# Performance work log

Measured on AMD Instinct MI355X. Metric: run time of the kernel, lower is better.

Reference implementation:

```python
import jax, jax.numpy as jnp
import numpy as np

N = 100000        # nodes
E = 3200000       # edges (before self loops)
DIN = 128         # dim_input
DOUT = 64         # dim_output
HID = 4           # per-head hidden of conv1
HEADS = 8         # num_in_head
G = 64            # number of graphs in the batch
NEG_SLOPE = 0.2   # PyG GATConv default


def _gat_conv(x, edge_index, W, att_src, att_dst, bias, concat):
    """PyG GATConv (add_self_loops=True, dropout inactive / eval mode)."""
    n = x.shape[0]
    heads, dout = att_src.shape
    h = (x @ W).reshape(n, heads, dout)                  # [N, H, F]
    loop = jnp.arange(n)
    src = jnp.concatenate([edge_index[0], loop])          # [Et]
    dst = jnp.concatenate([edge_index[1], loop])          # [Et]
    a_s = (h * att_src).sum(-1)                           # [N, H]
    a_d = (h * att_dst).sum(-1)                           # [N, H]
    alpha = jax.nn.leaky_relu(a_s[src] + a_d[dst], NEG_SLOPE)   # [Et, H]
    amax = jax.ops.segment_max(alpha, dst, num_segments=n)      # softmax over in-edges
    ex = jnp.exp(alpha - amax[dst])
    denom = jax.ops.segment_sum(ex, dst, num_segments=n)
    w = ex / (denom[dst] + 1e-16)                         # [Et, H]
    out = jax.ops.segment_sum(h[src] * w[:, :, None], dst, num_segments=n)  # [N, H, F]
    out = out.reshape(n, heads * dout) if concat else out.mean(axis=1)
    return out + bias


def setup_inputs() -> dict:
    key = jax.random.key(0)
    ks = jax.random.split(key, 11)
    x = jax.random.normal(ks[0], (N, DIN), jnp.float32)
    edge_index = jax.random.randint(ks[1], (2, E), 0, N)
    batch = jnp.sort(jax.random.randint(ks[2], (N,), 0, G))
    s1 = 1.0 / np.sqrt(DIN)
    W1 = jax.random.uniform(ks[3], (DIN, HEADS * HID), jnp.float32, -s1, s1)
    att_src1 = jax.random.normal(ks[4], (HEADS, HID), jnp.float32) * 0.1
    att_dst1 = jax.random.normal(ks[5], (HEADS, HID), jnp.float32) * 0.1
    b1 = jnp.zeros((HEADS * HID,), jnp.float32)
    s2 = 1.0 / np.sqrt(HEADS * HID)
    W2 = jax.random.uniform(ks[6], (HEADS * HID, DOUT), jnp.float32, -s2, s2)
    att_src2 = jax.random.normal(ks[7], (1, DOUT), jnp.float32) * 0.1
    att_dst2 = jax.random.normal(ks[8], (1, DOUT), jnp.float32) * 0.1
    b2 = jnp.zeros((DOUT,), jnp.float32)
    return {"x": x, "edge_index": edge_index, "batch": batch,
            "W1": W1, "att_src1": att_src1, "att_dst1": att_dst1, "b1": b1,
            "W2": W2, "att_src2": att_src2, "att_dst2": att_dst2, "b2": b2}


def reference(x, edge_index, batch, W1, att_src1, att_dst1, b1,
              W2, att_src2, att_dst2, b2):
    h = _gat_conv(x, edge_index, W1, att_src1, att_dst1, b1, concat=True)
    h = jax.nn.elu(h)
    h = _gat_conv(h, edge_index, W2, att_src2, att_dst2, b2, concat=False)
    # global_mean_pool over batch ids
    sums = jax.ops.segment_sum(h, batch, num_segments=G)          # [G, DOUT]
    counts = jax.ops.segment_sum(jnp.ones((N,), h.dtype), batch, num_segments=G)
    return sums / jnp.maximum(counts, 1.0)[:, None]
```

## Files before the change

### kernel.cpp

```cpp
#include <hip/hip_runtime.h>
#include <math.h>

static constexpr int NN   = 100000;
static constexpr int NE   = 3200000;
static constexpr int ET   = NE + NN;
static constexpr int DIN  = 128;
static constexpr int H1   = 8;
static constexpr int C1   = 32;
static constexpr int DOUT = 64;
static constexpr int NG   = 64;
static constexpr int NB_SCAN = (NN + 255) / 256;
static constexpr int SLAB = (NN + 255) / 256;
static constexpr int NODES_PER_XCD = (NN + 7) / 8;
static constexpr int SC_SLABS = (ET + 255) / 256;

__device__ __forceinline__ float lrelu(float x){ return x > 0.f ? x : 0.2f*x; }
__device__ __forceinline__ float bfl(unsigned int u){ return __uint_as_float(u << 16); }
__device__ __forceinline__ float bfh(unsigned int u){ return __uint_as_float(u & 0xffff0000u); }
__device__ __forceinline__ unsigned short f2bf(float x){
  unsigned int u = __float_as_uint(x);
  u += 0x7fffu + ((u >> 16) & 1u);
  return (unsigned short)(u >> 16);
}

__global__ __launch_bounds__(256) void k_gemm1(const float* __restrict__ x,
                                               const float* __restrict__ W,
                                               const float* __restrict__ as1,
                                               const float* __restrict__ ad1,
                                               unsigned short* __restrict__ h1b,
                                               float* __restrict__ a_s,
                                               float* __restrict__ a_d){
  __shared__ float w[DIN * C1];
  for (int i = threadIdx.x; i < DIN * C1; i += 256) w[i] = W[i];
  __syncthreads();
  int idx = blockIdx.x * 256 + threadIdx.x;
  int n = idx >> 5, j = idx & 31;
  const float* xr = x + (size_t)n * DIN;
  float acc = 0.f;
  #pragma unroll
  for (int k = 0; k < DIN; ++k) acc += xr[k] * w[k * C1 + j];
  h1b[idx] = f2bf(acc);
  float s = acc * as1[j], d = acc * ad1[j];
  s += __shfl_xor(s, 1, 64); s += __shfl_xor(s, 2, 64);
  d += __shfl_xor(d, 1, 64); d += __shfl_xor(d, 2, 64);
  if ((j & 3) == 0){ a_s[n * H1 + (j >> 2)] = s; a_d[n * H1 + (j >> 2)] = d; }
}

__global__ __launch_bounds__(256) void k_init_cnt(int* __restrict__ cnt){
  int n = blockIdx.x * 256 + threadIdx.x;
  if (n < NN) cnt[n] = 1;
}

__global__ __launch_bounds__(256) void k_hist8(const int* __restrict__ ei, int* __restrict__ cnt){
  int xcd = blockIdx.x & 7;
  int e = (blockIdx.x >> 3) * 256 + threadIdx.x;
  int d = ei[NE + e];
  if (d / NODES_PER_XCD == xcd) atomicAdd(&cnt[d], 1);
}

__global__ __launch_bounds__(256) void k_scan_blk(const int* __restrict__ cnt,
                                                  int* __restrict__ tmp, int* __restrict__ btot){
  int g = blockIdx.x * 256 + threadIdx.x;
  int v = (g < NN) ? cnt[g] : 0;
  int lane = threadIdx.x & 63, wv = threadIdx.x >> 6;
  int xv = v;
  #pragma unroll
  for (int o = 1; o < 64; o <<= 1){ int y = __shfl_up(xv, o, 64); if (lane >= o) xv += y; }
  __shared__ int ws[4];
  if (lane == 63) ws[wv] = xv;
  __syncthreads();
  int off = 0;
  for (int i = 0; i < wv; ++i) off += ws[i];
  xv += off;
  if (g < NN) tmp[g] = xv;
  if (threadIdx.x == 255) btot[blockIdx.x] = xv;
}

__global__ __launch_bounds__(512) void k_scan_top(int* __restrict__ btot){
  int t = threadIdx.x;
  int v = (t < NB_SCAN) ? btot[t] : 0;
  int lane = t & 63, wv = t >> 6;
  int xv = v;
  #pragma unroll
  for (int o = 1; o < 64; o <<= 1){ int y = __shfl_up(xv, o, 64); if (lane >= o) xv += y; }
  __shared__ int ws[8];
  if (lane == 63) ws[wv] = xv;
  __syncthreads();
  int off = 0;
  for (int i = 0; i < wv; ++i) off += ws[i];
  xv += off;
  if (t < NB_SCAN) btot[t] = xv - v;
}

__global__ __launch_bounds__(256) void k_scan_fin(const int* __restrict__ cnt,
                                                  const int* __restrict__ tmp,
                                                  const int* __restrict__ btot,
                                                  int* __restrict__ row, int* __restrict__ cur){
  int g = blockIdx.x * 256 + threadIdx.x;
  if (g < NN){
    int ex = tmp[g] - cnt[g] + btot[g >> 8];
    row[g] = ex; cur[g] = ex;
  } else if (g == NN){
    row[NN] = ET;
  }
}

__global__ __launch_bounds__(256) void k_scatter8(const int* __restrict__ ei,
                                                  int* __restrict__ cur, int* __restrict__ ssrc){
  int xcd = blockIdx.x & 7;
  int e = (blockIdx.x >> 3) * 256 + threadIdx.x;
  if (e >= ET) return;
  int s, d;
  if (e < NE) { s = ei[e]; d = ei[NE + e]; }
  else        { s = e - NE; d = s; }
  if (d / NODES_PER_XCD != xcd) return;
  int pos = atomicAdd(&cur[d], 1);
  ssrc[pos] = s;
}

__global__ __launch_bounds__(256, 4) void k_agg1(const int* __restrict__ row,
                                              const int* __restrict__ ssrc,
                                              const float* __restrict__ a_s,
                                              const float* __restrict__ a_d,
                                              const unsigned short* __restrict__ h1b,
                                              const float* __restrict__ b1,
                                              float* __restrict__ out1){
  int node = (blockIdx.x * 256 + threadIdx.x) >> 6;
  int lane = threadIdx.x & 63;
  int l = lane & 7, g = lane >> 3;
  float adv = a_d[node * H1 + l];
  int beg = row[node], end = row[node + 1];
  float a0 = 0.f, a1 = 0.f, a2 = 0.f, a3 = 0.f, den = 0.f;
  for (int base = beg; base < end; base += 64){
    int sv[8]; float liv[8];
    #pragma unroll
    for (int u = 0; u < 8; ++u){
      int k = base + u * 8 + g;
      liv[u] = (k < end) ? 1.f : 0.f;
      sv[u] = ssrc[k < end ? k : end - 1];
    }
    uint2 hraw[8]; float araw[8];
    #pragma unroll
    for (int u = 0; u < 8; ++u){
      hraw[u] = *(const uint2*)(h1b + (size_t)sv[u] * C1 + 4 * l);
      araw[u] = a_s[sv[u] * H1 + l];
    }
    #pragma unroll
    for (int u = 0; u < 8; ++u){
      float al = liv[u] * __expf(lrelu(araw[u] + adv));
      den += al;
      a0 += al * bfl(hraw[u].x); a1 += al * bfh(hraw[u].x);
      a2 += al * bfl(hraw[u].y); a3 += al * bfh(hraw[u].y);
    }
  }
  #pragma unroll
  for (int o = 8; o < 64; o <<= 1){
    den += __shfl_xor(den, o, 64);
    a0 += __shfl_xor(a0, o, 64); a1 += __shfl_xor(a1, o, 64);
    a2 += __shfl_xor(a2, o, 64); a3 += __shfl_xor(a3, o, 64);
  }
  if (g == 0){
    float r = 1.f / den;
    float4 bv = *(const float4*)(b1 + 4 * l);
    float v0 = a0 * r + bv.x, v1 = a1 * r + bv.y, v2 = a2 * r + bv.z, v3 = a3 * r + bv.w;
    v0 = v0 > 0.f ? v0 : expm1f(v0); v1 = v1 > 0.f ? v1 : expm1f(v1);
    v2 = v2 > 0.f ? v2 : expm1f(v2); v3 = v3 > 0.f ? v3 : expm1f(v3);
    *(float4*)(out1 + (size_t)node * C1 + 4 * l) = make_float4(v0, v1, v2, v3);
  }
}

__global__ __launch_bounds__(256) void k_gemm2(const float* __restrict__ hin,
                                               const float* __restrict__ W,
                                               const float* __restrict__ as2,
                                               const float* __restrict__ ad2,
                                               unsigned short* __restrict__ h2b,
                                               float* __restrict__ a_s,
                                               float* __restrict__ a_d){
  __shared__ float w[C1 * DOUT];
  for (int i = threadIdx.x; i < C1 * DOUT; i += 256) w[i] = W[i];
  __syncthreads();
  int idx = blockIdx.x * 256 + threadIdx.x;
  int n = idx >> 6, j = idx & 63;
  const float* hr = hin + (size_t)n * C1;
  float acc = 0.f;
  #pragma unroll
  for (int k = 0; k < C1; ++k) acc += hr[k] * w[k * DOUT + j];
  h2b[idx] = f2bf(acc);
  float s = acc * as2[j], d = acc * ad2[j];
  #pragma unroll
  for (int o = 1; o < 64; o <<= 1){ s += __shfl_xor(s, o, 64); d += __shfl_xor(d, o, 64); }
  if (j == 0){ a_s[n] = s; a_d[n] = d; }
}

__global__ __launch_bounds__(256, 4) void k_agg2(const int* __restrict__ row,
                                              const int* __restrict__ ssrc,
                                              const float* __restrict__ a_s,
                                              const float* __restrict__ a_d,
                                              const unsigned short* __restrict__ h2b,
                                              float* __restrict__ out2){
  int node = (blockIdx.x * 256 + threadIdx.x) >> 6;
  int lane = threadIdx.x & 63;
  int l = lane & 15, g = lane >> 4;
  float adv = a_d[node];
  int beg = row[node], end = row[node + 1];
  float ac0 = 0.f, ac1 = 0.f, ac2 = 0.f, ac3 = 0.f, den = 0.f;
  for (int base = beg; base < end; base += 32){
    int sv[8]; float liv[8];
    #pragma unroll
    for (int u = 0; u < 8; ++u){
      int k = base + u * 4 + g;
      liv[u] = (k < end) ? 1.f : 0.f;
      sv[u] = ssrc[k < end ? k : end - 1];
    }
    uint2 hraw[8]; float asv[8];
    #pragma unroll
    for (int u = 0; u < 8; ++u){
      hraw[u] = *(const uint2*)(h2b + (size_t)sv[u] * DOUT + 4 * l);
      asv[u] = a_s[sv[u]];
    }
    #pragma unroll
    for (int u = 0; u < 8; ++u){
      float al = liv[u] * __expf(lrelu(asv[u] + adv));
      den += al;
      ac0 += al * bfl(hraw[u].x); ac1 += al * bfh(hraw[u].x);
      ac2 += al * bfl(hraw[u].y); ac3 += al * bfh(hraw[u].y);
    }
  }
  #pragma unroll
  for (int o = 16; o < 64; o <<= 1){
    den += __shfl_xor(den, o, 64);
    ac0 += __shfl_xor(ac0, o, 64); ac1 += __shfl_xor(ac1, o, 64);
    ac2 += __shfl_xor(ac2, o, 64); ac3 += __shfl_xor(ac3, o, 64);
  }
  if (g == 0){
    float r = 1.f / den;
    *(float4*)(out2 + (size_t)node * DOUT + 4 * l) =
        make_float4(ac0 * r, ac1 * r, ac2 * r, ac3 * r);
  }
}

__global__ __launch_bounds__(256) void k_bounds(const int* __restrict__ batch,
                                                int* __restrict__ gs){
  int n = blockIdx.x * 256 + threadIdx.x;
  if (n >= NN) return;
  int b = batch[n];
  if (n == 0) gs[b] = 0;
  else if (batch[n - 1] != b) gs[b] = n;
}

__global__ void k_fix(int* __restrict__ gs){
  if (threadIdx.x == 0){
    gs[NG] = NN;
    for (int g = NG - 1; g >= 0; --g) if (gs[g] < 0) gs[g] = gs[g + 1];
  }
}

__global__ __launch_bounds__(256) void k_pool(const float* __restrict__ out2,
                                              const int* __restrict__ batch,
                                              float* __restrict__ sums){
  int start = blockIdx.x * SLAB;
  int stop  = start + SLAB; if (stop > NN) stop = NN;
  int wv = threadIdx.x >> 6, lane = threadIdx.x & 63;
  int n0 = start + wv;
  if (n0 >= stop) return;
  float acc = 0.f;
  int cur_g = batch[n0];
  for (int n = n0; n < stop; n += 4){
    int g = batch[n];
    if (g != cur_g){
      atomicAdd(&sums[cur_g * DOUT + lane], acc);
      acc = 0.f; cur_g = g;
    }
    acc += out2[(size_t)n * DOUT + lane];
  }
  atomicAdd(&sums[cur_g * DOUT + lane], acc);
}

__global__ __launch_bounds__(256) void k_final(const float* __restrict__ sums,
                                               const int* __restrict__ gs,
                                               const float* __restrict__ b2,
                                               float* __restrict__ out){
  int idx = blockIdx.x * 256 + threadIdx.x;
  if (idx >= NG * DOUT) return;
  int g = idx >> 6, f = idx & 63;
  int c = gs[g + 1] - gs[g];
  out[idx] = sums[idx] / (float)(c > 0 ? c : 1) + b2[f];
}

extern "C" void kernel_launch(void* const* d_in, const int* in_sizes, int n_in,
                              void* d_out, int out_size, void* d_ws, size_t ws_size,
                              hipStream_t stream) {
  const float* x   = (const float*)d_in[0];
  const int*   ei  = (const int*)  d_in[1];
  const int*   bat = (const int*)  d_in[2];
  const float* W1  = (const float*)d_in[3];
  const float* as1 = (const float*)d_in[4];
  const float* ad1 = (const float*)d_in[5];
  const float* b1  = (const float*)d_in[6];
  const float* W2  = (const float*)d_in[7];
  const float* as2 = (const float*)d_in[8];
  const float* ad2 = (const float*)d_in[9];
  const float* b2  = (const float*)d_in[10];
  float* out = (float*)d_out;

  char* p = (char*)d_ws;
  auto alloc = [&](size_t bytes){ void* r = p; p += (bytes + 255) & ~(size_t)255; return r; };
  unsigned short* h1b  = (unsigned short*)alloc((size_t)NN * C1 * 2);
  float* a_s1  = (float*)alloc((size_t)NN * H1 * 4);
  float* a_d1  = (float*)alloc((size_t)NN * H1 * 4);
  float* out1  = (float*)alloc((size_t)NN * C1 * 4);
  unsigned short* h2b  = (unsigned short*)alloc((size_t)NN * DOUT * 2);
  float* a_s2  = (float*)alloc(NN * 4);
  float* a_d2  = (float*)alloc(NN * 4);
  float* out2  = (float*)alloc((size_t)NN * DOUT * 4);
  int*   row   = (int*)alloc((NN + 1) * 4);
  int*   cur   = (int*)alloc(NN * 4);
  int*   tmp   = (int*)alloc(NN * 4);
  int*   btot  = (int*)alloc(512 * 4);
  int*   cnt   = (int*)alloc(NN * 4);
  int*   ssrc  = (int*)alloc((size_t)ET * 4);
  float* sums  = (float*)alloc(NG * DOUT * 4);
  int*   gs    = (int*)alloc((NG + 1) * 4);

  hipMemsetAsync(sums, 0, NG * DOUT * 4, stream);
  hipMemsetAsync(gs, 0xFF, (NG + 1) * 4, stream);
  k_init_cnt<<<(NN + 255) / 256, 256, 0, stream>>>(cnt);

  k_gemm1<<<(NN * C1) / 256, 256, 0, stream>>>(x, W1, as1, ad1, h1b, a_s1, a_d1);

  k_hist8   <<<(NE / 256) * 8, 256, 0, stream>>>(ei, cnt);
  k_scan_blk<<<NB_SCAN, 256, 0, stream>>>(cnt, tmp, btot);
  k_scan_top<<<1, 512, 0, stream>>>(btot);
  k_scan_fin<<<(NN + 256) / 256, 256, 0, stream>>>(cnt, tmp, btot, row, cur);
  k_scatter8<<<SC_SLABS * 8, 256, 0, stream>>>(ei, cur, ssrc);

  k_bounds<<<(NN + 255) / 256, 256, 0, stream>>>(bat, gs);
  k_fix<<<1, 64, 0, stream>>>(gs);

  k_agg1<<<(NN * 64) / 256, 256, 0, stream>>>(row, ssrc, a_s1, a_d1, h1b, b1, out1);

  k_gemm2<<<(NN * DOUT) / 256, 256, 0, stream>>>(out1, W2, as2, ad2, h2b, a_s2, a_d2);
  k_agg2 <<<(NN * 64) / 256, 256, 0, stream>>>(row, ssrc, a_s2, a_d2, h2b, out2);

  k_pool <<<256, 256, 0, stream>>>(out2, bat, sums);
  k_final<<<(NG * DOUT + 255) / 256, 256, 0, stream>>>(sums, gs, b2, out);
}
```

Before: 675.1 us.

## Use nontemporal loads/stores on streaming data and defer source index reads

Marks streaming reads (x, edge dst/src, ssrc, out2) and the stores of out1/out2 as nontemporal so they pollute cache less. The scatter kernel now reads the source index only for edges owned by the current XCD, which removes redundant src reads across the 8 replicated passes. The count-init kernel is replaced by a memset to zero, with the self-loop +1 folded into the scan. Nontemporal hints on data that is reused, such as ssrc across both aggregations and out1 read by gemm2, could lower cache hit rates.

```diff
diff --git a/kernel.cpp b/kernel.cpp
--- a/kernel.cpp
+++ b/kernel.cpp
@@ -13,6 +13,8 @@
 static constexpr int SLAB = (NN + 255) / 256;
 static constexpr int NODES_PER_XCD = (NN + 7) / 8;
 static constexpr int SC_SLABS = (ET + 255) / 256;
+
+using fx4 = __attribute__((ext_vector_type(4))) float;
 
 __device__ __forceinline__ float lrelu(float x){ return x > 0.f ? x : 0.2f*x; }
 __device__ __forceinline__ float bfl(unsigned int u){ return __uint_as_float(u << 16); }
@@ -38,7 +40,7 @@
   const float* xr = x + (size_t)n * DIN;
   float acc = 0.f;
   #pragma unroll
-  for (int k = 0; k < DIN; ++k) acc += xr[k] * w[k * C1 + j];
+  for (int k = 0; k < DIN; ++k) acc += __builtin_nontemporal_load(xr + k) * w[k * C1 + j];
   h1b[idx] = f2bf(acc);
   float s = acc * as1[j], d = acc * ad1[j];
   s += __shfl_xor(s, 1, 64); s += __shfl_xor(s, 2, 64);
@@ -46,22 +48,17 @@
   if ((j & 3) == 0){ a_s[n * H1 + (j >> 2)] = s; a_d[n * H1 + (j >> 2)] = d; }
 }
 
-__global__ __launch_bounds__(256) void k_init_cnt(int* __restrict__ cnt){
-  int n = blockIdx.x * 256 + threadIdx.x;
-  if (n < NN) cnt[n] = 1;
-}
-
 __global__ __launch_bounds__(256) void k_hist8(const int* __restrict__ ei, int* __restrict__ cnt){
   int xcd = blockIdx.x & 7;
   int e = (blockIdx.x >> 3) * 256 + threadIdx.x;
-  int d = ei[NE + e];
+  int d = __builtin_nontemporal_load(ei + NE + e);
   if (d / NODES_PER_XCD == xcd) atomicAdd(&cnt[d], 1);
 }
 
 __global__ __launch_bounds__(256) void k_scan_blk(const int* __restrict__ cnt,
                                                   int* __restrict__ tmp, int* __restrict__ btot){
   int g = blockIdx.x * 256 + threadIdx.x;
-  int v = (g < NN) ? cnt[g] : 0;
+  int v = (g < NN) ? cnt[g] + 1 : 0;
   int lane = threadIdx.x & 63, wv = threadIdx.x >> 6;
   int xv = v;
   #pragma unroll
@@ -98,7 +95,7 @@
                                                   int* __restrict__ row, int* __restrict__ cur){
   int g = blockIdx.x * 256 + threadIdx.x;
   if (g < NN){
-    int ex = tmp[g] - cnt[g] + btot[g >> 8];
+    int ex = tmp[g] - (cnt[g] + 1) + btot[g >> 8];
     row[g] = ex; cur[g] = ex;
   } else if (g == NN){
     row[NN] = ET;
@@ -111,9 +108,10 @@
   int e = (blockIdx.x >> 3) * 256 + threadIdx.x;
   if (e >= ET) return;
   int s, d;
-  if (e < NE) { s = ei[e]; d = ei[NE + e]; }
+  if (e < NE) { d = __builtin_nontemporal_load(ei + NE + e); s = -1; }
   else        { s = e - NE; d = s; }
   if (d / NODES_PER_XCD != xcd) return;
+  if (s < 0) s = __builtin_nontemporal_load(ei + e);
   int pos = atomicAdd(&cur[d], 1);
   ssrc[pos] = s;
 }
@@ -137,7 +135,7 @@
     for (int u = 0; u < 8; ++u){
       int k = base + u * 8 + g;
       liv[u] = (k < end) ? 1.f : 0.f;
-      sv[u] = ssrc[k < end ? k : end - 1];
+      sv[u] = __builtin_nontemporal_load(ssrc + (k < end ? k : end - 1));
     }
     uint2 hraw[8]; float araw[8];
     #pragma unroll
@@ -165,7 +163,8 @@
     float v0 = a0 * r + bv.x, v1 = a1 * r + bv.y, v2 = a2 * r + bv.z, v3 = a3 * r + bv.w;
     v0 = v0 > 0.f ? v0 : expm1f(v0); v1 = v1 > 0.f ? v1 : expm1f(v1);
     v2 = v2 > 0.f ? v2 : expm1f(v2); v3 = v3 > 0.f ? v3 : expm1f(v3);
-    *(float4*)(out1 + (size_t)node * C1 + 4 * l) = make_float4(v0, v1, v2, v3);
+    fx4 o4; o4.x = v0; o4.y = v1; o4.z = v2; o4.w = v3;
+    __builtin_nontemporal_store(o4, (fx4*)(out1 + (size_t)node * C1 + 4 * l));
   }
 }
 
@@ -210,7 +209,7 @@
     for (int u = 0; u < 8; ++u){
       int k = base + u * 4 + g;
       liv[u] = (k < end) ? 1.f : 0.f;
-      sv[u] = ssrc[k < end ? k : end - 1];
+      sv[u] = __builtin_nontemporal_load(ssrc + (k < end ? k : end - 1));
     }
     uint2 hraw[8]; float asv[8];
     #pragma unroll
@@ -234,8 +233,8 @@
   }
   if (g == 0){
     float r = 1.f / den;
-    *(float4*)(out2 + (size_t)node * DOUT + 4 * l) =
-        make_float4(ac0 * r, ac1 * r, ac2 * r, ac3 * r);
+    fx4 o4; o4.x = ac0 * r; o4.y = ac1 * r; o4.z = ac2 * r; o4.w = ac3 * r;
+    __builtin_nontemporal_store(o4, (fx4*)(out2 + (size_t)node * DOUT + 4 * l));
   }
 }
 
@@ -271,7 +270,7 @@
       atomicAdd(&sums[cur_g * DOUT + lane], acc);
       acc = 0.f; cur_g = g;
     }
-    acc += out2[(size_t)n * DOUT + lane];
+    acc += __builtin_nontemporal_load(out2 + (size_t)n * DOUT + lane);
   }
   atomicAdd(&sums[cur_g * DOUT + lane], acc);
 }
@@ -324,7 +323,7 @@
 
   hipMemsetAsync(sums, 0, NG * DOUT * 4, stream);
   hipMemsetAsync(gs, 0xFF, (NG + 1) * 4, stream);
-  k_init_cnt<<<(NN + 255) / 256, 256, 0, stream>>>(cnt);
+  hipMemsetAsync(cnt, 0, NN * 4, stream);
 
   k_gemm1<<<(NN * C1) / 256, 256, 0, stream>>>(x, W1, as1, ad1, h1b, a_s1, a_d1);
 
```

Result: slower. 717.2 us (+6.2%).
